# Optimization experiments

Hardware: AMD Instinct MI355X
Metric: run time of the kernel (lower is better)

Reference implementation:

```python
import jax, jax.numpy as jnp
import numpy as np
import math

S = 10      # fixed sequence length
D = 128     # hidden dim


def _position():
    j = np.arange(D // 2)
    i = np.arange(S)[:, None]
    ang = i / np.power(1000.0, 2.0 * j / D)
    pos = np.zeros((S, D), dtype=np.float32)
    pos[:, 0::2] = np.sin(ang)
    pos[:, 1::2] = np.cos(ang)
    return jnp.asarray(pos)


def _mask():
    # mask[j, i] = -inf when i < j (strict lower triangle of original torch mask)
    r = np.arange(S)
    m = np.where(r[None, :] < r[:, None], -np.inf, 0.0).astype(np.float32)
    return jnp.asarray(m)


POS = _position()
MASK = _mask()
INV_SQRT10 = np.float32(1.0 / math.sqrt(10.0))


def setup_inputs() -> dict:
    key = jax.random.key(0)
    ks = jax.random.split(key, 16)
    B = 32768
    f = jax.random.normal
    return {
        "x": f(ks[0], (B, S, 4), dtype=jnp.float32),
        "L_w": f(ks[1], (4, D), dtype=jnp.float32),
        "UL_w": f(ks[2], (D, 4), dtype=jnp.float32),
        "WQ": f(ks[3], (D, 64), dtype=jnp.float32),
        "WK": f(ks[4], (D, 64), dtype=jnp.float32),
        "WVd": f(ks[5], (D, 64), dtype=jnp.float32),
        "WVu": f(ks[6], (64, D), dtype=jnp.float32),
        "WQ2": f(ks[7], (D, 64), dtype=jnp.float32),
        "WK2": f(ks[8], (D, 64), dtype=jnp.float32),
        "WVd2": f(ks[9], (D, 64), dtype=jnp.float32),
        "WVu2": f(ks[10], (64, D), dtype=jnp.float32),
        "quesin": f(ks[11], (S, D, 64), dtype=jnp.float32),
        "quesout": f(ks[12], (S, 64, D), dtype=jnp.float32),
        "quesin2": f(ks[13], (S, D, 64), dtype=jnp.float32),
        "quesout2": f(ks[14], (S, 64, D), dtype=jnp.float32),
    }


def _attn_block(h, WQ, WK, WVd, WVu):
    # h: [B, S, D]
    Q = h @ WQ                               # [B, S, 64]
    K = h @ WK                               # [B, S, 64]
    V = (h @ WVd) @ WVu                      # [B, S, D]
    # C[n, j, i] = sum_k Q[n,i,k] K[n,j,k]; mask added per batch; softmax over axis 1 (j)
    C = jnp.einsum('nik,njk->nji', Q, K) + MASK[None]
    C = jax.nn.softmax(C, axis=1)
    # DE[n, k, j] = sum_i V[n,i,j] C[n,i,k]
    DE = jnp.einsum('nij,nik->nkj', V, C)
    return h + DE * INV_SQRT10


def reference(x, L_w, UL_w, WQ, WK, WVd, WVu, WQ2, WK2, WVd2, WVu2,
              quesin, quesout, quesin2, quesout2):
    h = x @ L_w + POS                        # [B, S, D]
    E2 = _attn_block(h, WQ, WK, WVd, WVu)
    # per-position low-rank projection: [B,S,D] x [S,D,64] x [S,64,D] -> [B,S,D]
    h = jnp.einsum('mnj,nji,nik->mnk', E2, quesin, quesout)
    E22 = _attn_block(h, WQ2, WK2, WVd2, WVu2)
    h = jnp.einsum('mnj,nji,nik->mnk', E22, quesin2, quesout2)
    return h @ UL_w                          # [B, S, 4]
```

## Files before the change

### kernel.cpp

```cpp
#include <hip/hip_runtime.h>
#include <math.h>

#define TS 10
#define TD 128
#define TE 64
#define BT 8
#define NTHR 256
#define HSTR 132
#define QSTR 68
#define NHROWS (TS*BT)

#define HS_FLOATS (NHROWS*HSTR)
#define BUF_FLOATS (40*QSTR)
#define P_FLOATS (BT*TS*12)
#define LDS_FLOATS (HS_FLOATS + 3*BUF_FLOATS + P_FLOATS)

#define INVSQRT10 0.31622776601683794f

#define WS_POS   0
#define WS_LW    1280
#define WS_PW    2048
#define WS_ZW    3968
#define WS_LQ    6528
#define WS_PQ    9088
#define WS_ZQ    9728
#define WS_WVUQ  12288
#define WS_W2N   53248

typedef float v2f __attribute__((ext_vector_type(2)));

#define PKFMA_LO(acc_, ap_, wp_) \
    asm("v_pk_fma_f32 %0, %1, %2, %0 op_sel:[0,0,0] op_sel_hi:[0,1,1]" \
        : "+v"(acc_) : "v"(ap_), "v"(wp_))
#define PKFMA_HI(acc_, ap_, wp_) \
    asm("v_pk_fma_f32 %0, %1, %2, %0 op_sel:[1,0,0] op_sel_hi:[1,1,1]" \
        : "+v"(acc_) : "v"(ap_), "v"(wp_))

#define WSYNC() do { __builtin_amdgcn_wave_barrier(); \
    asm volatile("s_waitcnt lgkmcnt(0)" ::: "memory"); \
    __builtin_amdgcn_wave_barrier(); } while (0)

__device__ __forceinline__ float pos_val(int n, int d) {
    int j = d >> 1;
    double ang = (double)n / pow(1000.0, 2.0 * (double)j / (double)TD);
    return (float)((d & 1) ? cos(ang) : sin(ang));
}

__global__ void pre_kernel(float* __restrict__ ws,
                           const float* __restrict__ L_w,
                           const float* __restrict__ WQ,
                           const float* __restrict__ WK,
                           const float* __restrict__ WVd,
                           const float* __restrict__ qin2,
                           const float* __restrict__ qout2,
                           const float* __restrict__ UL_w,
                           const float* __restrict__ WVu2,
                           const float* __restrict__ qin1,
                           const float* __restrict__ WVu,
                           const float* __restrict__ qout1,
                           const float* __restrict__ WQ2,
                           const float* __restrict__ WK2,
                           const float* __restrict__ WVd2) {
    const int tid = threadIdx.x;
    const int bid = blockIdx.x;

    if (bid == 0) {
        __shared__ float sPOS[TS * TD];
        for (int idx = tid; idx < TS * TD; idx += 256) {
            float v = pos_val(idx / TD, idx % TD);
            sPOS[idx] = v;
            ws[WS_POS + idx] = v;
        }
        __syncthreads();
        for (int idx = tid; idx < 3 * 4 * TE; idx += 256) {
            int p = idx >> 8, r = idx & 255, c = r >> 6, e = r & 63;
            const float* Wp = (p == 0 ? WQ : (p == 1 ? WK : WVd));
            const float* lr = L_w + c * TD;
            float acc = 0.f;
            for (int d = 0; d < TD; d++) acc = fmaf(lr[d], Wp[d * TE + e], acc);
            ws[WS_LW + idx] = acc;
        }
        for (int idx = tid; idx < 3 * TS * TE; idx += 256) {
            int p = idx / 640, r = idx % 640, n = r >> 6, e = r & 63;
            const float* Wp = (p == 0 ? WQ : (p == 1 ? WK : WVd));
            const float* pr = sPOS + n * TD;
            float acc = 0.f;
            for (int d = 0; d < TD; d++) acc = fmaf(pr[d], Wp[d * TE + e], acc);
            ws[WS_PW + idx] = acc;
        }
        return;
    }
    if (bid <= 10) {
        int n = bid - 1;
        __shared__ float sQ[TD * TE];
        __shared__ float sPOSn[TD];
        for (int idx = tid; idx < TD * TE / 4; idx += 256)
            *(float4*)(sQ + idx * 4) =
                *(const float4*)(qin1 + (size_t)n * TD * TE + idx * 4);
        if (tid < TD) sPOSn[tid] = pos_val(n, tid);
        __syncthreads();
        for (int t = tid; t < 320; t += 256) {
            if (t < 256) {
                int c = t >> 6, k = t & 63;
                const float* lr = L_w + c * TD;
                float acc = 0.f;
                for (int d = 0; d < TD; d++) acc = fmaf(lr[d], sQ[d * TE + k], acc);
                ws[WS_LQ + n * 256 + t] = acc;
            } else {
                int k = t - 256;
                float acc = 0.f;
                for (int d = 0; d < TD; d++) acc = fmaf(sPOSn[d], sQ[d * TE + k], acc);
                ws[WS_PQ + n * TE + k] = acc;
            }
        }
        float* dst = ws + WS_WVUQ + n * 4096;
        for (int idx = tid; idx < TE * TE; idx += 256) {
            int e = idx >> 6, k = idx & 63;
            const float* wv = WVu + (size_t)e * TD;
            float acc = 0.f;
            for (int d = 0; d < TD; d += 4) {
                float4 w4 = *(const float4*)(wv + d);
                acc = fmaf(w4.x, sQ[(d + 0) * TE + k], acc);
                acc = fmaf(w4.y, sQ[(d + 1) * TE + k], acc);
                acc = fmaf(w4.z, sQ[(d + 2) * TE + k], acc);
                acc = fmaf(w4.w, sQ[(d + 3) * TE + k], acc);
            }
            dst[idx] = acc;
        }
        return;
    }
    if (bid <= 70) {
        int t = bid - 11;
        int half = t & 1, pn = t >> 1;
        int p = pn / 10, n = pn % 10;
        const float* Wp = (p == 0 ? WQ2 : (p == 1 ? WK2 : WVd2));
        float* dst = ws + WS_W2N + (pn << 12);
        for (int idx = tid; idx < 2048; idx += 256) {
            int k = half * 32 + (idx >> 6), e = idx & 63;
            const float* qp = qout1 + ((size_t)n * TE + k) * TD;
            float acc = 0.f;
            for (int j = 0; j < TD; j += 4) {
                float4 q4 = *(const float4*)(qp + j);
                acc = fmaf(q4.x, Wp[(j + 0) * TE + e], acc);
                acc = fmaf(q4.y, Wp[(j + 1) * TE + e], acc);
                acc = fmaf(q4.z, Wp[(j + 2) * TE + e], acc);
                acc = fmaf(q4.w, Wp[(j + 3) * TE + e], acc);
            }
            dst[k * TE + e] = acc;
        }
        return;
    }
    {
        int t = bid - 71, n = t >> 2, c = t & 3;
        __shared__ float sP2r[TE];
        __shared__ float sZr[TD];
        if (tid < TE) {
            int i = tid;
            const float* qp = qout2 + ((size_t)n * TE + i) * TD;
            float acc = 0.f;
            for (int d = 0; d < TD; d += 4) {
                float4 q4 = *(const float4*)(qp + d);
                acc = fmaf(q4.x, UL_w[(d + 0) * 4 + c], acc);
                acc = fmaf(q4.y, UL_w[(d + 1) * 4 + c], acc);
                acc = fmaf(q4.z, UL_w[(d + 2) * 4 + c], acc);
                acc = fmaf(q4.w, UL_w[(d + 3) * 4 + c], acc);
            }
            sP2r[i] = acc;
        }
        __syncthreads();
        if (tid < TD) {
            int j = tid;
            const float* ip = qin2 + ((size_t)n * TD + j) * TE;
            float acc = 0.f;
            for (int i = 0; i < TE; i += 4) {
                float4 q4 = *(const float4*)(ip + i);
                acc = fmaf(q4.x, sP2r[i + 0], acc);
                acc = fmaf(q4.y, sP2r[i + 1], acc);
                acc = fmaf(q4.z, sP2r[i + 2], acc);
                acc = fmaf(q4.w, sP2r[i + 3], acc);
            }
            sZr[j] = acc;
        }
        __syncthreads();
        if (tid < TE) {
            int e = tid;
            const float* wp = WVu2 + (size_t)e * TD;
            float acc = 0.f;
            for (int j = 0; j < TD; j += 4) {
                float4 w4 = *(const float4*)(wp + j);
                acc = fmaf(w4.x, sZr[j + 0], acc);
                acc = fmaf(w4.y, sZr[j + 1], acc);
                acc = fmaf(w4.z, sZr[j + 2], acc);
                acc = fmaf(w4.w, sZr[j + 3], acc);
            }
            ws[WS_ZW + (n * 4 + c) * TE + e] = acc;
        } else if (tid < 2 * TE) {
            int k = tid - TE;
            const float* qp = qout1 + ((size_t)n * TE + k) * TD;
            float acc = 0.f;
            for (int j = 0; j < TD; j += 4) {
                float4 q4 = *(const float4*)(qp + j);
                acc = fmaf(q4.x, sZr[j + 0], acc);
                acc = fmaf(q4.y, sZr[j + 1], acc);
                acc = fmaf(q4.z, sZr[j + 2], acc);
                acc = fmaf(q4.w, sZr[j + 3], acc);
            }
            ws[WS_ZQ + (n * 4 + c) * TE + k] = acc;
        }
    }
}

template <int M, int SPLIT, int C, int K, bool ADD>
__device__ __forceinline__ void gemm_f32(
    const float* __restrict__ Ap, int a0, int aHi, int aLo,
    const float* __restrict__ W, int ws,
    float* __restrict__ Op, int o0, int oHi, int oLo,
    float scale)
{
    static_assert(C % 4 == 0, "C must be a multiple of 4");
    static_assert(K % 16 == 0 && K >= 32, "K must be a multiple of 16, >=32");
    constexpr int CG = C / 4;
    constexpr int CP = C / 2;
    v2f acc[M][CP];
#pragma unroll
    for (int m = 0; m < M; m++)
#pragma unroll
        for (int p = 0; p < CP; p++) acc[m][p] = (v2f)(0.f);

    float4 aR0[M], aR1[M];
    float4 wA[8 * CG], wB[8 * CG];
    const float* ap = Ap + a0;
    const float* wp = W;

    auto loadW8 = [&](float4* wR, const float* w) {
#pragma unroll
        for (int kk = 0; kk < 8; kk++)
#pragma unroll
            for (int cg = 0; cg < CG; cg++)
                wR[kk * CG + cg] = *(const float4*)(w + kk * ws + cg * 4);
    };
    auto loadA = [&](float4* aR, const float* a) {
#pragma unroll
        for (int m = 0; m < M; m++)
            aR[m] = *(const float4*)(a + (m / SPLIT) * aHi + (m % SPLIT) * aLo);
    };
    auto computeH = [&](const float4* aR, const float4* wR) {
#pragma unroll
        for (int m = 0; m < M; m++) {
            const v2f* ap2 = (const v2f*)&aR[m];
#pragma unroll
            for (int kp = 0; kp < 2; kp++) {
                const v2f* wf0 = (const v2f*)&wR[(2 * kp + 0) * CG];
                const v2f* wf1 = (const v2f*)&wR[(2 * kp + 1) * CG];
#pragma unroll
                for (int p = 0; p < CP; p++) {
                    PKFMA_LO(acc[m][p], ap2[kp], wf0[p]);
                    PKFMA_HI(acc[m][p], ap2[kp], wf1[p]);
                }
            }
        }
    };

    loadW8(wA, wp);
    loadA(aR0, ap);
#pragma unroll 1
    for (int k = 0; k + 16 < K; k += 16) {
        loadW8(wB, wp + 8 * ws);
        loadA(aR1, ap + 4);
        computeH(aR0, wA);
        loadA(aR0, ap + 8);
        computeH(aR1, wA + 4 * CG);
        loadW8(wA, wp + 16 * ws);
        loadA(aR1, ap + 12);
        computeH(aR0, wB);
        loadA(aR0, ap + 16);
        computeH(aR1, wB + 4 * CG);
        wp += 16 * ws; ap += 16;
    }
    loadW8(wB, wp + 8 * ws);
    loadA(aR1, ap + 4);
    computeH(aR0, wA);
    loadA(aR0, ap + 8);
    computeH(aR1, wA + 4 * CG);
    loadA(aR1, ap + 12);
    computeH(aR0, wB);
    computeH(aR1, wB + 4 * CG);

    v2f s2; s2.x = scale; s2.y = scale;
#pragma unroll
    for (int m = 0; m < M; m++) {
        float* op = Op + o0 + (m / SPLIT) * oHi + (m % SPLIT) * oLo;
#pragma unroll
        for (int cg = 0; cg < CG; cg++) {
            float4 r;
            v2f* rp = (v2f*)&r;
            if constexpr (ADD) {
                float4 v = *(float4*)(op + cg * 4);
                const v2f* vp = (const v2f*)&v;
                rp[0] = s2 * acc[m][cg * 2 + 0] + vp[0];
                rp[1] = s2 * acc[m][cg * 2 + 1] + vp[1];
            } else {
                rp[0] = s2 * acc[m][cg * 2 + 0];
                rp[1] = s2 * acc[m][cg * 2 + 1];
            }
            *(float4*)(op + cg * 4) = r;
        }
    }
}

extern "C" __global__ __launch_bounds__(NTHR, 2)
void trans_fused(const float* __restrict__ x,
                 const float* __restrict__ L_w, const float* __restrict__ UL_w,
                 const float* __restrict__ WQ,  const float* __restrict__ WK,
                 const float* __restrict__ WVd, const float* __restrict__ WVu,
                 const float* __restrict__ WQ2, const float* __restrict__ WK2,
                 const float* __restrict__ WVd2,const float* __restrict__ WVu2,
                 const float* __restrict__ qin1,const float* __restrict__ qout1,
                 const float* __restrict__ qin2,const float* __restrict__ qout2,
                 const float* __restrict__ POSb, float* __restrict__ out)
{
    extern __shared__ float lds[];
    float* Hs = lds;
    float* Qb = lds + HS_FLOATS;
    float* Kb = Qb + BUF_FLOATS;
    float* Vb = Kb + BUF_FLOATS;
    float* Pb = Vb + BUF_FLOATS;

    const int tid = threadIdx.x;
    const int vtid = (tid + ((blockIdx.x & 3) << 6)) & 255;
    const int w = vtid >> 6;
    const int l = vtid & 63;
    const int gb0 = blockIdx.x * BT;
    const float* LWb   = POSb + WS_LW;
    const float* PWb   = POSb + WS_PW;
    const float* ZWb   = POSb + WS_ZW;
    const float* LQb   = POSb + WS_LQ;
    const float* PQb   = POSb + WS_PQ;
    const float* ZQb   = POSb + WS_ZQ;
    const float* WVuQb = POSb + WS_WVUQ;
    const float* W2Nb  = POSb + WS_W2N;

    for (int hb = 0; hb < 2; ++hb) {
        for (int t = vtid; t < 2560; t += NTHR) {
            if (t < 1920) {
                int p = t / 640, r2 = t % 640, rr = r2 >> 4, e4 = r2 & 15;
                int b4 = rr / 10, n = rr - b4 * 10;
                const float* xp = x + ((size_t)(gb0 + hb * 4 + b4) * TS + n) * 4;
                float4 x4 = *(const float4*)xp;
                const float* xf = (const float*)&x4;
                const float* lw = LWb + p * 256 + e4 * 4;
                float4 pw = *(const float4*)(PWb + p * 640 + n * 64 + e4 * 4);
                v2f a0 = ((const v2f*)&pw)[0], a1 = ((const v2f*)&pw)[1];
#pragma unroll
                for (int c = 0; c < 4; c++) {
                    float4 l4 = *(const float4*)(lw + c * 64);
                    v2f xb; xb.x = xf[c]; xb.y = xf[c];
                    a0 = xb * ((const v2f*)&l4)[0] + a0;
                    a1 = xb * ((const v2f*)&l4)[1] + a1;
                }
                float* Ob = (p == 0 ? Qb : (p == 1 ? Kb : Vb));
                float4 r4;
                ((v2f*)&r4)[0] = a0; ((v2f*)&r4)[1] = a1;
                *(float4*)(Ob + rr * QSTR + e4 * 4) = r4;
            } else {
                int t2 = t - 1920;
                int rr = t2 >> 4, cg = t2 & 15;
                int b4 = rr / 10, n = rr - b4 * 10;
                const float* xp = x + ((size_t)(gb0 + hb * 4 + b4) * TS + n) * 4;
                float4 x4 = *(const float4*)xp;
                const float* xf = (const float*)&x4;
                const float* lq = LQb + n * 256 + cg * 4;
                float4 pq = *(const float4*)(PQb + n * 64 + cg * 4);
                v2f a0 = ((const v2f*)&pq)[0], a1 = ((const v2f*)&pq)[1];
#pragma unroll
                for (int c = 0; c < 4; c++) {
                    float4 l4 = *(const float4*)(lq + c * 64);
                    v2f xb; xb.x = xf[c]; xb.y = xf[c];
                    a0 = xb * ((const v2f*)&l4)[0] + a0;
                    a1 = xb * ((const v2f*)&l4)[1] + a1;
                }
                float4 r4;
                ((v2f*)&r4)[0] = a0; ((v2f*)&r4)[1] = a1;
                *(float4*)(Hs + (hb * 40 + rr) * HSTR + cg * 4) = r4;
            }
        }
        __syncthreads();

        if (l < 55) {
            int i = 0, base = 0, pr = l;
            while (pr >= base + i + 1) { base += i + 1; i++; }
            int j = pr - base;
            const float* qr = Qb + (w * 10 + i) * QSTR;
            const float* kr = Kb + (w * 10 + j) * QSTR;
            v2f s0 = (v2f)(0.f), s1 = (v2f)(0.f);
            for (int e = 0; e < TE; e += 8) {
                float4 qa = *(const float4*)(qr + e);
                float4 ka = *(const float4*)(kr + e);
                float4 qc = *(const float4*)(qr + e + 4);
                float4 kc = *(const float4*)(kr + e + 4);
                s0 = ((const v2f*)&qa)[0] * ((const v2f*)&ka)[0] + s0;
                s1 = ((const v2f*)&qa)[1] * ((const v2f*)&ka)[1] + s1;
                s0 = ((const v2f*)&qc)[0] * ((const v2f*)&kc)[0] + s0;
                s1 = ((const v2f*)&qc)[1] * ((const v2f*)&kc)[1] + s1;
            }
            Pb[(hb * 4 + w) * 120 + i * 12 + j] = (s0.x + s0.y) + (s1.x + s1.y);
        }
        WSYNC();

        if (l < TS) {
            float* pr = Pb + (hb * 4 + w) * 120 + l * 12;
            float m = pr[0];
#pragma unroll
            for (int j = 1; j < TS; j++) if (j <= l) m = fmaxf(m, pr[j]);
            float sum = 0.f;
#pragma unroll
            for (int j = 0; j < TS; j++) if (j <= l) { float e = expf(pr[j] - m); pr[j] = e; sum += e; }
#pragma unroll
            for (int j = 0; j < TS; j++) pr[j] = (j <= l) ? pr[j] / sum : 0.f;
        }
        WSYNC();

        for (int oi = l; oi < 160; oi += 64) {
            int q = oi >> 4, e4 = (oi & 15) * 4;
            const float* pp = Pb + (hb * 4 + w) * 120 + q * 12;
            v2f g0 = (v2f)(0.f), g1 = (v2f)(0.f);
#pragma unroll
            for (int k = 0; k < TS; k++) {
                float p = pp[k];
                v2f pv; pv.x = p; pv.y = p;
                float4 v = *(const float4*)(Vb + (w * 10 + k) * QSTR + e4);
                g0 = pv * ((const v2f*)&v)[0] + g0;
                g1 = pv * ((const v2f*)&v)[1] + g1;
            }
            float4 g;
            ((v2f*)&g)[0] = g0; ((v2f*)&g)[1] = g1;
            *(float4*)(Qb + (w * 10 + q) * QSTR + e4) = g;
        }
        __syncthreads();

        if (vtid < 160) {
            int n = vtid >> 4, cg = vtid & 15;
            gemm_f32<4, 1, 4, TE, true>(
                Qb, n * QSTR, 10 * QSTR, 0,
                WVuQb + n * 4096 + cg * 4, TE,
                Hs, (hb * 40 + n) * HSTR + cg * 4, 10 * HSTR, 0,
                INVSQRT10);
        }
        __syncthreads();
    }

    for (int hb = 0; hb < 2; ++hb) {
        for (int t = vtid; t < 480; t += NTHR) {
            int p = t / 160, rem = t - p * 160, n = rem >> 4, cg = rem & 15;
            float* Ob = (p == 0 ? Qb : (p == 1 ? Kb : Vb));
            gemm_f32<4, 1, 4, TE, false>(
                Hs, (hb * 40 + n) * HSTR, 10 * HSTR, 0,
                W2Nb + ((p * 10 + n) << 12) + cg * 4, TE,
                Ob, n * QSTR + cg * 4, 10 * QSTR, 0, 1.f);
        }
        __syncthreads();

        if (l < 55) {
            int i = 0, base = 0, pr = l;
            while (pr >= base + i + 1) { base += i + 1; i++; }
            int j = pr - base;
            const float* qr = Qb + (w * 10 + i) * QSTR;
            const float* kr = Kb + (w * 10 + j) * QSTR;
            v2f s0 = (v2f)(0.f), s1 = (v2f)(0.f);
            for (int e = 0; e < TE; e += 8) {
                float4 qa = *(const float4*)(qr + e);
                float4 ka = *(const float4*)(kr + e);
                float4 qc = *(const float4*)(qr + e + 4);
                float4 kc = *(const float4*)(kr + e + 4);
                s0 = ((const v2f*)&qa)[0] * ((const v2f*)&ka)[0] + s0;
                s1 = ((const v2f*)&qa)[1] * ((const v2f*)&ka)[1] + s1;
                s0 = ((const v2f*)&qc)[0] * ((const v2f*)&kc)[0] + s0;
                s1 = ((const v2f*)&qc)[1] * ((const v2f*)&kc)[1] + s1;
            }
            Pb[(hb * 4 + w) * 120 + i * 12 + j] = (s0.x + s0.y) + (s1.x + s1.y);
        }
        WSYNC();

        if (l < TS) {
            float* pr = Pb + (hb * 4 + w) * 120 + l * 12;
            float m = pr[0];
#pragma unroll
            for (int j = 1; j < TS; j++) if (j <= l) m = fmaxf(m, pr[j]);
            float sum = 0.f;
#pragma unroll
            for (int j = 0; j < TS; j++) if (j <= l) { float e = expf(pr[j] - m); pr[j] = e; sum += e; }
#pragma unroll
            for (int j = 0; j < TS; j++) pr[j] = (j <= l) ? pr[j] / sum : 0.f;
        }
        WSYNC();

        for (int oi = l; oi < 160; oi += 64) {
            int q = oi >> 4, e4 = (oi & 15) * 4;
            const float* pp = Pb + (hb * 4 + w) * 120 + q * 12;
            v2f g0 = (v2f)(0.f), g1 = (v2f)(0.f);
#pragma unroll
            for (int k = 0; k < TS; k++) {
                float p = pp[k];
                v2f pv; pv.x = p; pv.y = p;
                float4 v = *(const float4*)(Vb + (w * 10 + k) * QSTR + e4);
                g0 = pv * ((const v2f*)&v)[0] + g0;
                g1 = pv * ((const v2f*)&v)[1] + g1;
            }
            float4 g;
            ((v2f*)&g)[0] = g0; ((v2f*)&g)[1] = g1;
            *(float4*)(Qb + (w * 10 + q) * QSTR + e4) = g;
        }
        WSYNC();

        if (l < 40) {
            int n = l >> 2, c = l & 3;
            const float* tr = Hs + (hb * 40 + w * 10 + n) * HSTR;
            const float* zq = ZQb + (n * 4 + c) * TE;
            v2f s0 = (v2f)(0.f), s1 = (v2f)(0.f);
            for (int k = 0; k < TE; k += 8) {
                float4 ta = *(const float4*)(tr + k);
                float4 za = *(const float4*)(zq + k);
                float4 tc = *(const float4*)(tr + k + 4);
                float4 zc = *(const float4*)(zq + k + 4);
                s0 = ((const v2f*)&ta)[0] * ((const v2f*)&za)[0] + s0;
                s1 = ((const v2f*)&ta)[1] * ((const v2f*)&za)[1] + s1;
                s0 = ((const v2f*)&tc)[0] * ((const v2f*)&zc)[0] + s0;
                s1 = ((const v2f*)&tc)[1] * ((const v2f*)&zc)[1] + s1;
            }
            float base = (s0.x + s0.y) + (s1.x + s1.y);
            const float* gr = Qb + (w * 10 + n) * QSTR;
            const float* zw = ZWb + (n * 4 + c) * TE;
            v2f a0 = (v2f)(0.f), a1 = (v2f)(0.f);
            for (int e = 0; e < TE; e += 8) {
                float4 ga = *(const float4*)(gr + e);
                float4 za = *(const float4*)(zw + e);
                float4 gc = *(const float4*)(gr + e + 4);
                float4 zc = *(const float4*)(zw + e + 4);
                a0 = ((const v2f*)&ga)[0] * ((const v2f*)&za)[0] + a0;
                a1 = ((const v2f*)&ga)[1] * ((const v2f*)&za)[1] + a1;
                a0 = ((const v2f*)&gc)[0] * ((const v2f*)&zc)[0] + a0;
                a1 = ((const v2f*)&gc)[1] * ((const v2f*)&zc)[1] + a1;
            }
            float att = (a0.x + a0.y) + (a1.x + a1.y);
            out[((size_t)(gb0 + hb * 4 + w) * TS + n) * 4 + c] =
                base + att * INVSQRT10;
        }
        __syncthreads();
    }
}

extern "C" void kernel_launch(void* const* d_in, const int* in_sizes, int n_in,
                              void* d_out, int out_size, void* d_ws, size_t ws_size,
                              hipStream_t stream) {
    const float* x    = (const float*)d_in[0];
    const float* L_w  = (const float*)d_in[1];
    const float* UL_w = (const float*)d_in[2];
    const float* WQ   = (const float*)d_in[3];
    const float* WK   = (const float*)d_in[4];
    const float* WVd  = (const float*)d_in[5];
    const float* WVu  = (const float*)d_in[6];
    const float* WQ2  = (const float*)d_in[7];
    const float* WK2  = (const float*)d_in[8];
    const float* WVd2 = (const float*)d_in[9];
    const float* WVu2 = (const float*)d_in[10];
    const float* qin1 = (const float*)d_in[11];
    const float* qout1= (const float*)d_in[12];
    const float* qin2 = (const float*)d_in[13];
    const float* qout2= (const float*)d_in[14];
    float* out = (float*)d_out;
    float* POSb = (float*)d_ws;

    int B = in_sizes[0] / (TS * 4);
    size_t lds_bytes = (size_t)LDS_FLOATS * sizeof(float);

    (void)hipFuncSetAttribute((const void*)trans_fused,
                              hipFuncAttributeMaxDynamicSharedMemorySize,
                              (int)lds_bytes);

    pre_kernel<<<dim3(111), dim3(256), 0, stream>>>(
        POSb, L_w, WQ, WK, WVd, qin2, qout2, UL_w, WVu2, qin1, WVu,
        qout1, WQ2, WK2, WVd2);
    trans_fused<<<dim3(B / BT), dim3(NTHR), lds_bytes, stream>>>(
        x, L_w, UL_w, WQ, WK, WVd, WVu, WQ2, WK2, WVd2, WVu2,
        qin1, qout1, qin2, qout2, POSb, out);
}
```

Measured before the change: 615.8 us.

## Process four batches per block instead of eight and shrink H tile stride

Halves the batch tile per workgroup from 8 to 4, removing the two-pass half-batch loops so each block handles a single group of four sequences. The H buffer row stride drops from 132 to 68 floats, so the LDS footprint shrinks, which is meant to let more workgroups reside per CU. The grid doubles, so per-block overhead and weight reloads from global/L2 are paid twice as often.

```diff
diff --git a/kernel.cpp b/kernel.cpp
--- a/kernel.cpp
+++ b/kernel.cpp
@@ -4,9 +4,9 @@
 #define TS 10
 #define TD 128
 #define TE 64
-#define BT 8
+#define BT 4
 #define NTHR 256
-#define HSTR 132
+#define HSTR 68
 #define QSTR 68
 #define NHROWS (TS*BT)
 
@@ -340,212 +340,206 @@
     const float* WVuQb = POSb + WS_WVUQ;
     const float* W2Nb  = POSb + WS_W2N;
 
-    for (int hb = 0; hb < 2; ++hb) {
-        for (int t = vtid; t < 2560; t += NTHR) {
-            if (t < 1920) {
-                int p = t / 640, r2 = t % 640, rr = r2 >> 4, e4 = r2 & 15;
-                int b4 = rr / 10, n = rr - b4 * 10;
-                const float* xp = x + ((size_t)(gb0 + hb * 4 + b4) * TS + n) * 4;
-                float4 x4 = *(const float4*)xp;
-                const float* xf = (const float*)&x4;
-                const float* lw = LWb + p * 256 + e4 * 4;
-                float4 pw = *(const float4*)(PWb + p * 640 + n * 64 + e4 * 4);
-                v2f a0 = ((const v2f*)&pw)[0], a1 = ((const v2f*)&pw)[1];
-#pragma unroll
-                for (int c = 0; c < 4; c++) {
-                    float4 l4 = *(const float4*)(lw + c * 64);
-                    v2f xb; xb.x = xf[c]; xb.y = xf[c];
-                    a0 = xb * ((const v2f*)&l4)[0] + a0;
-                    a1 = xb * ((const v2f*)&l4)[1] + a1;
-                }
-                float* Ob = (p == 0 ? Qb : (p == 1 ? Kb : Vb));
-                float4 r4;
-                ((v2f*)&r4)[0] = a0; ((v2f*)&r4)[1] = a1;
-                *(float4*)(Ob + rr * QSTR + e4 * 4) = r4;
-            } else {
-                int t2 = t - 1920;
-                int rr = t2 >> 4, cg = t2 & 15;
-                int b4 = rr / 10, n = rr - b4 * 10;
-                const float* xp = x + ((size_t)(gb0 + hb * 4 + b4) * TS + n) * 4;
-                float4 x4 = *(const float4*)xp;
-                const float* xf = (const float*)&x4;
-                const float* lq = LQb + n * 256 + cg * 4;
-                float4 pq = *(const float4*)(PQb + n * 64 + cg * 4);
-                v2f a0 = ((const v2f*)&pq)[0], a1 = ((const v2f*)&pq)[1];
-#pragma unroll
-                for (int c = 0; c < 4; c++) {
-                    float4 l4 = *(const float4*)(lq + c * 64);
-                    v2f xb; xb.x = xf[c]; xb.y = xf[c];
-                    a0 = xb * ((const v2f*)&l4)[0] + a0;
-                    a1 = xb * ((const v2f*)&l4)[1] + a1;
-                }
-                float4 r4;
-                ((v2f*)&r4)[0] = a0; ((v2f*)&r4)[1] = a1;
-                *(float4*)(Hs + (hb * 40 + rr) * HSTR + cg * 4) = r4;
-            }
-        }
-        __syncthreads();
-
-        if (l < 55) {
-            int i = 0, base = 0, pr = l;
-            while (pr >= base + i + 1) { base += i + 1; i++; }
-            int j = pr - base;
-            const float* qr = Qb + (w * 10 + i) * QSTR;
-            const float* kr = Kb + (w * 10 + j) * QSTR;
-            v2f s0 = (v2f)(0.f), s1 = (v2f)(0.f);
-            for (int e = 0; e < TE; e += 8) {
-                float4 qa = *(const float4*)(qr + e);
-                float4 ka = *(const float4*)(kr + e);
-                float4 qc = *(const float4*)(qr + e + 4);
-                float4 kc = *(const float4*)(kr + e + 4);
-                s0 = ((const v2f*)&qa)[0] * ((const v2f*)&ka)[0] + s0;
-                s1 = ((const v2f*)&qa)[1] * ((const v2f*)&ka)[1] + s1;
-                s0 = ((const v2f*)&qc)[0] * ((const v2f*)&kc)[0] + s0;
-                s1 = ((const v2f*)&qc)[1] * ((const v2f*)&kc)[1] + s1;
-            }
-            Pb[(hb * 4 + w) * 120 + i * 12 + j] = (s0.x + s0.y) + (s1.x + s1.y);
-        }
-        WSYNC();
-
-        if (l < TS) {
-            float* pr = Pb + (hb * 4 + w) * 120 + l * 12;
-            float m = pr[0];
-#pragma unroll
-            for (int j = 1; j < TS; j++) if (j <= l) m = fmaxf(m, pr[j]);
-            float sum = 0.f;
-#pragma unroll
-            for (int j = 0; j < TS; j++) if (j <= l) { float e = expf(pr[j] - m); pr[j] = e; sum += e; }
-#pragma unroll
-            for (int j = 0; j < TS; j++) pr[j] = (j <= l) ? pr[j] / sum : 0.f;
-        }
-        WSYNC();
-
-        for (int oi = l; oi < 160; oi += 64) {
-            int q = oi >> 4, e4 = (oi & 15) * 4;
-            const float* pp = Pb + (hb * 4 + w) * 120 + q * 12;
-            v2f g0 = (v2f)(0.f), g1 = (v2f)(0.f);
-#pragma unroll
-            for (int k = 0; k < TS; k++) {
-                float p = pp[k];
-                v2f pv; pv.x = p; pv.y = p;
-                float4 v = *(const float4*)(Vb + (w * 10 + k) * QSTR + e4);
-                g0 = pv * ((const v2f*)&v)[0] + g0;
-                g1 = pv * ((const v2f*)&v)[1] + g1;
-            }
-            float4 g;
-            ((v2f*)&g)[0] = g0; ((v2f*)&g)[1] = g1;
-            *(float4*)(Qb + (w * 10 + q) * QSTR + e4) = g;
-        }
-        __syncthreads();
-
-        if (vtid < 160) {
-            int n = vtid >> 4, cg = vtid & 15;
-            gemm_f32<4, 1, 4, TE, true>(
-                Qb, n * QSTR, 10 * QSTR, 0,
-                WVuQb + n * 4096 + cg * 4, TE,
-                Hs, (hb * 40 + n) * HSTR + cg * 4, 10 * HSTR, 0,
-                INVSQRT10);
-        }
-        __syncthreads();
-    }
-
-    for (int hb = 0; hb < 2; ++hb) {
-        for (int t = vtid; t < 480; t += NTHR) {
-            int p = t / 160, rem = t - p * 160, n = rem >> 4, cg = rem & 15;
+    for (int t = vtid; t < 2560; t += NTHR) {
+        if (t < 1920) {
+            int p = t / 640, r2 = t % 640, rr = r2 >> 4, e4 = r2 & 15;
+            int b4 = rr / 10, n = rr - b4 * 10;
+            const float* xp = x + ((size_t)(gb0 + b4) * TS + n) * 4;
+            float4 x4 = *(const float4*)xp;
+            const float* xf = (const float*)&x4;
+            const float* lw = LWb + p * 256 + e4 * 4;
+            float4 pw = *(const float4*)(PWb + p * 640 + n * 64 + e4 * 4);
+            v2f a0 = ((const v2f*)&pw)[0], a1 = ((const v2f*)&pw)[1];
+#pragma unroll
+            for (int c = 0; c < 4; c++) {
+                float4 l4 = *(const float4*)(lw + c * 64);
+                v2f xb; xb.x = xf[c]; xb.y = xf[c];
+                a0 = xb * ((const v2f*)&l4)[0] + a0;
+                a1 = xb * ((const v2f*)&l4)[1] + a1;
+            }
             float* Ob = (p == 0 ? Qb : (p == 1 ? Kb : Vb));
-            gemm_f32<4, 1, 4, TE, false>(
-                Hs, (hb * 40 + n) * HSTR, 10 * HSTR, 0,
-                W2Nb + ((p * 10 + n) << 12) + cg * 4, TE,
-                Ob, n * QSTR + cg * 4, 10 * QSTR, 0, 1.f);
-        }
-        __syncthreads();
-
-        if (l < 55) {
-            int i = 0, base = 0, pr = l;
-            while (pr >= base + i + 1) { base += i + 1; i++; }
-            int j = pr - base;
-            const float* qr = Qb + (w * 10 + i) * QSTR;
-            const float* kr = Kb + (w * 10 + j) * QSTR;
-            v2f s0 = (v2f)(0.f), s1 = (v2f)(0.f);
-            for (int e = 0; e < TE; e += 8) {
-                float4 qa = *(const float4*)(qr + e);
-                float4 ka = *(const float4*)(kr + e);
-                float4 qc = *(const float4*)(qr + e + 4);
-                float4 kc = *(const float4*)(kr + e + 4);
-                s0 = ((const v2f*)&qa)[0] * ((const v2f*)&ka)[0] + s0;
-                s1 = ((const v2f*)&qa)[1] * ((const v2f*)&ka)[1] + s1;
-                s0 = ((const v2f*)&qc)[0] * ((const v2f*)&kc)[0] + s0;
-                s1 = ((const v2f*)&qc)[1] * ((const v2f*)&kc)[1] + s1;
-            }
-            Pb[(hb * 4 + w) * 120 + i * 12 + j] = (s0.x + s0.y) + (s1.x + s1.y);
-        }
-        WSYNC();
-
-        if (l < TS) {
-            float* pr = Pb + (hb * 4 + w) * 120 + l * 12;
-            float m = pr[0];
-#pragma unroll
-            for (int j = 1; j < TS; j++) if (j <= l) m = fmaxf(m, pr[j]);
-            float sum = 0.f;
-#pragma unroll
-            for (int j = 0; j < TS; j++) if (j <= l) { float e = expf(pr[j] - m); pr[j] = e; sum += e; }
-#pragma unroll
-            for (int j = 0; j < TS; j++) pr[j] = (j <= l) ? pr[j] / sum : 0.f;
-        }
-        WSYNC();
-
-        for (int oi = l; oi < 160; oi += 64) {
-            int q = oi >> 4, e4 = (oi & 15) * 4;
-            const float* pp = Pb + (hb * 4 + w) * 120 + q * 12;
-            v2f g0 = (v2f)(0.f), g1 = (v2f)(0.f);
-#pragma unroll
-            for (int k = 0; k < TS; k++) {
-                float p = pp[k];
-                v2f pv; pv.x = p; pv.y = p;
-                float4 v = *(const float4*)(Vb + (w * 10 + k) * QSTR + e4);
-                g0 = pv * ((const v2f*)&v)[0] + g0;
-                g1 = pv * ((const v2f*)&v)[1] + g1;
-            }
-            float4 g;
-            ((v2f*)&g)[0] = g0; ((v2f*)&g)[1] = g1;
-            *(float4*)(Qb + (w * 10 + q) * QSTR + e4) = g;
-        }
-        WSYNC();
-
-        if (l < 40) {
-            int n = l >> 2, c = l & 3;
-            const float* tr = Hs + (hb * 40 + w * 10 + n) * HSTR;
-            const float* zq = ZQb + (n * 4 + c) * TE;
-            v2f s0 = (v2f)(0.f), s1 = (v2f)(0.f);
-            for (int k = 0; k < TE; k += 8) {
-                float4 ta = *(const float4*)(tr + k);
-                float4 za = *(const float4*)(zq + k);
-                float4 tc = *(const float4*)(tr + k + 4);
-                float4 zc = *(const float4*)(zq + k + 4);
-                s0 = ((const v2f*)&ta)[0] * ((const v2f*)&za)[0] + s0;
-                s1 = ((const v2f*)&ta)[1] * ((const v2f*)&za)[1] + s1;
-                s0 = ((const v2f*)&tc)[0] * ((const v2f*)&zc)[0] + s0;
-                s1 = ((const v2f*)&tc)[1] * ((const v2f*)&zc)[1] + s1;
-            }
-            float base = (s0.x + s0.y) + (s1.x + s1.y);
-            const float* gr = Qb + (w * 10 + n) * QSTR;
-            const float* zw = ZWb + (n * 4 + c) * TE;
-            v2f a0 = (v2f)(0.f), a1 = (v2f)(0.f);
-            for (int e = 0; e < TE; e += 8) {
-                float4 ga = *(const float4*)(gr + e);
-                float4 za = *(const float4*)(zw + e);
-                float4 gc = *(const float4*)(gr + e + 4);
-                float4 zc = *(const float4*)(zw + e + 4);
-                a0 = ((const v2f*)&ga)[0] * ((const v2f*)&za)[0] + a0;
-                a1 = ((const v2f*)&ga)[1] * ((const v2f*)&za)[1] + a1;
-                a0 = ((const v2f*)&gc)[0] * ((const v2f*)&zc)[0] + a0;
-                a1 = ((const v2f*)&gc)[1] * ((const v2f*)&zc)[1] + a1;
-            }
-            float att = (a0.x + a0.y) + (a1.x + a1.y);
-            out[((size_t)(gb0 + hb * 4 + w) * TS + n) * 4 + c] =
-                base + att * INVSQRT10;
-        }
-        __syncthreads();
+            float4 r4;
+            ((v2f*)&r4)[0] = a0; ((v2f*)&r4)[1] = a1;
+            *(float4*)(Ob + rr * QSTR + e4 * 4) = r4;
+        } else {
+            int t2 = t - 1920;
+            int rr = t2 >> 4, cg = t2 & 15;
+            int b4 = rr / 10, n = rr - b4 * 10;
+            const float* xp = x + ((size_t)(gb0 + b4) * TS + n) * 4;
+            float4 x4 = *(const float4*)xp;
+            const float* xf = (const float*)&x4;
+            const float* lq = LQb + n * 256 + cg * 4;
+            float4 pq = *(const float4*)(PQb + n * 64 + cg * 4);
+            v2f a0 = ((const v2f*)&pq)[0], a1 = ((const v2f*)&pq)[1];
+#pragma unroll
+            for (int c = 0; c < 4; c++) {
+                float4 l4 = *(const float4*)(lq + c * 64);
+                v2f xb; xb.x = xf[c]; xb.y = xf[c];
+                a0 = xb * ((const v2f*)&l4)[0] + a0;
+                a1 = xb * ((const v2f*)&l4)[1] + a1;
+            }
+            float4 r4;
+            ((v2f*)&r4)[0] = a0; ((v2f*)&r4)[1] = a1;
+            *(float4*)(Hs + rr * HSTR + cg * 4) = r4;
+        }
+    }
+    __syncthreads();
+
+    if (l < 55) {
+        int i = 0, base = 0, pr = l;
+        while (pr >= base + i + 1) { base += i + 1; i++; }
+        int j = pr - base;
+        const float* qr = Qb + (w * 10 + i) * QSTR;
+        const float* kr = Kb + (w * 10 + j) * QSTR;
+        v2f s0 = (v2f)(0.f), s1 = (v2f)(0.f);
+        for (int e = 0; e < TE; e += 8) {
+            float4 qa = *(const float4*)(qr + e);
+            float4 ka = *(const float4*)(kr + e);
+            float4 qc = *(const float4*)(qr + e + 4);
+            float4 kc = *(const float4*)(kr + e + 4);
+            s0 = ((const v2f*)&qa)[0] * ((const v2f*)&ka)[0] + s0;
+            s1 = ((const v2f*)&qa)[1] * ((const v2f*)&ka)[1] + s1;
+            s0 = ((const v2f*)&qc)[0] * ((const v2f*)&kc)[0] + s0;
+            s1 = ((const v2f*)&qc)[1] * ((const v2f*)&kc)[1] + s1;
+        }
+        Pb[w * 120 + i * 12 + j] = (s0.x + s0.y) + (s1.x + s1.y);
+    }
+    WSYNC();
+
+    if (l < TS) {
+        float* pr = Pb + w * 120 + l * 12;
+        float m = pr[0];
+#pragma unroll
+        for (int j = 1; j < TS; j++) if (j <= l) m = fmaxf(m, pr[j]);
+        float sum = 0.f;
+#pragma unroll
+        for (int j = 0; j < TS; j++) if (j <= l) { float e = expf(pr[j] - m); pr[j] = e; sum += e; }
+#pragma unroll
+        for (int j = 0; j < TS; j++) pr[j] = (j <= l) ? pr[j] / sum : 0.f;
+    }
+    WSYNC();
+
+    for (int oi = l; oi < 160; oi += 64) {
+        int q = oi >> 4, e4 = (oi & 15) * 4;
+        const float* pp = Pb + w * 120 + q * 12;
+        v2f g0 = (v2f)(0.f), g1 = (v2f)(0.f);
+#pragma unroll
+        for (int k = 0; k < TS; k++) {
+            float p = pp[k];
+            v2f pv; pv.x = p; pv.y = p;
+            float4 v = *(const float4*)(Vb + (w * 10 + k) * QSTR + e4);
+            g0 = pv * ((const v2f*)&v)[0] + g0;
+            g1 = pv * ((const v2f*)&v)[1] + g1;
+        }
+        float4 g;
+        ((v2f*)&g)[0] = g0; ((v2f*)&g)[1] = g1;
+        *(float4*)(Qb + (w * 10 + q) * QSTR + e4) = g;
+    }
+    __syncthreads();
+
+    if (vtid < 160) {
+        int n = vtid >> 4, cg = vtid & 15;
+        gemm_f32<4, 1, 4, TE, true>(
+            Qb, n * QSTR, 10 * QSTR, 0,
+            WVuQb + n * 4096 + cg * 4, TE,
+            Hs, n * HSTR + cg * 4, 10 * HSTR, 0,
+            INVSQRT10);
+    }
+    __syncthreads();
+
+    for (int t = vtid; t < 480; t += NTHR) {
+        int p = t / 160, rem = t - p * 160, n = rem >> 4, cg = rem & 15;
+        float* Ob = (p == 0 ? Qb : (p == 1 ? Kb : Vb));
+        gemm_f32<4, 1, 4, TE, false>(
+            Hs, n * HSTR, 10 * HSTR, 0,
+            W2Nb + ((p * 10 + n) << 12) + cg * 4, TE,
+            Ob, n * QSTR + cg * 4, 10 * QSTR, 0, 1.f);
+    }
+    __syncthreads();
+
+    if (l < 55) {
+        int i = 0, base = 0, pr = l;
+        while (pr >= base + i + 1) { base += i + 1; i++; }
+        int j = pr - base;
+        const float* qr = Qb + (w * 10 + i) * QSTR;
+        const float* kr = Kb + (w * 10 + j) * QSTR;
+        v2f s0 = (v2f)(0.f), s1 = (v2f)(0.f);
+        for (int e = 0; e < TE; e += 8) {
+            float4 qa = *(const float4*)(qr + e);
+            float4 ka = *(const float4*)(kr + e);
+            float4 qc = *(const float4*)(qr + e + 4);
+            float4 kc = *(const float4*)(kr + e + 4);
+            s0 = ((const v2f*)&qa)[0] * ((const v2f*)&ka)[0] + s0;
+            s1 = ((const v2f*)&qa)[1] * ((const v2f*)&ka)[1] + s1;
+            s0 = ((const v2f*)&qc)[0] * ((const v2f*)&kc)[0] + s0;
+            s1 = ((const v2f*)&qc)[1] * ((const v2f*)&kc)[1] + s1;
+        }
+        Pb[w * 120 + i * 12 + j] = (s0.x + s0.y) + (s1.x + s1.y);
+    }
+    WSYNC();
+
+    if (l < TS) {
+        float* pr = Pb + w * 120 + l * 12;
+        float m = pr[0];
+#pragma unroll
+        for (int j = 1; j < TS; j++) if (j <= l) m = fmaxf(m, pr[j]);
+        float sum = 0.f;
+#pragma unroll
+        for (int j = 0; j < TS; j++) if (j <= l) { float e = expf(pr[j] - m); pr[j] = e; sum += e; }
+#pragma unroll
+        for (int j = 0; j < TS; j++) pr[j] = (j <= l) ? pr[j] / sum : 0.f;
+    }
+    WSYNC();
+
+    for (int oi = l; oi < 160; oi += 64) {
+        int q = oi >> 4, e4 = (oi & 15) * 4;
+        const float* pp = Pb + w * 120 + q * 12;
+        v2f g0 = (v2f)(0.f), g1 = (v2f)(0.f);
+#pragma unroll
+        for (int k = 0; k < TS; k++) {
+            float p = pp[k];
+            v2f pv; pv.x = p; pv.y = p;
+            float4 v = *(const float4*)(Vb + (w * 10 + k) * QSTR + e4);
+            g0 = pv * ((const v2f*)&v)[0] + g0;
+            g1 = pv * ((const v2f*)&v)[1] + g1;
+        }
+        float4 g;
+        ((v2f*)&g)[0] = g0; ((v2f*)&g)[1] = g1;
+        *(float4*)(Qb + (w * 10 + q) * QSTR + e4) = g;
+    }
+    WSYNC();
+
+    if (l < 40) {
+        int n = l >> 2, c = l & 3;
+        const float* tr = Hs + (w * 10 + n) * HSTR;
+        const float* zq = ZQb + (n * 4 + c) * TE;
+        v2f s0 = (v2f)(0.f), s1 = (v2f)(0.f);
+        for (int k = 0; k < TE; k += 8) {
+            float4 ta = *(const float4*)(tr + k);
+            float4 za = *(const float4*)(zq + k);
+            float4 tc = *(const float4*)(tr + k + 4);
+            float4 zc = *(const float4*)(zq + k + 4);
+            s0 = ((const v2f*)&ta)[0] * ((const v2f*)&za)[0] + s0;
+            s1 = ((const v2f*)&ta)[1] * ((const v2f*)&za)[1] + s1;
+            s0 = ((const v2f*)&tc)[0] * ((const v2f*)&zc)[0] + s0;
+            s1 = ((const v2f*)&tc)[1] * ((const v2f*)&zc)[1] + s1;
+        }
+        float base = (s0.x + s0.y) + (s1.x + s1.y);
+        const float* gr = Qb + (w * 10 + n) * QSTR;
+        const float* zw = ZWb + (n * 4 + c) * TE;
+        v2f a0 = (v2f)(0.f), a1 = (v2f)(0.f);
+        for (int e = 0; e < TE; e += 8) {
+            float4 ga = *(const float4*)(gr + e);
+            float4 za = *(const float4*)(zw + e);
+            float4 gc = *(const float4*)(gr + e + 4);
+            float4 zc = *(const float4*)(zw + e + 4);
+            a0 = ((const v2f*)&ga)[0] * ((const v2f*)&za)[0] + a0;
+            a1 = ((const v2f*)&ga)[1] * ((const v2f*)&za)[1] + a1;
+            a0 = ((const v2f*)&gc)[0] * ((const v2f*)&zc)[0] + a0;
+            a1 = ((const v2f*)&gc)[1] * ((const v2f*)&zc)[1] + a1;
+        }
+        float att = (a0.x + a0.y) + (a1.x + a1.y);
+        out[((size_t)(gb0 + w) * TS + n) * 4 + c] = base + att * INVSQRT10;
     }
 }
 
```

Result: faster. 555.4 us (-9.8%).
